# Performance work log

Hardware: AMD Instinct MI355X
Metric: run time of the kernel (lower is better)

## Reference

```python
import jax, jax.numpy as jnp
import numpy as np

N_NODES = 50000
N_EDGES = 800000
N_GRAPHS = 64
IN_C, HID_C, OUT_C = 768, 128, 1


def setup_inputs() -> dict:
    key = jax.random.key(0)
    ks = jax.random.split(key, 9)
    x = jax.random.normal(ks[0], (N_NODES, IN_C), dtype=jnp.float32)
    edge_index = jax.random.randint(ks[1], (2, N_EDGES), 0, N_NODES, dtype=jnp.int32)
    batch = jnp.sort(jax.random.randint(ks[2], (N_NODES,), 0, N_GRAPHS, dtype=jnp.int32))
    s1 = 1.0 / np.sqrt(IN_C)
    s2 = 1.0 / np.sqrt(HID_C)
    W1 = jax.random.normal(ks[3], (IN_C, HID_C), dtype=jnp.float32) * s1
    b1 = jnp.zeros((HID_C,), dtype=jnp.float32)
    W2 = jax.random.normal(ks[4], (HID_C, HID_C), dtype=jnp.float32) * s2
    b2 = jnp.zeros((HID_C,), dtype=jnp.float32)
    Wl = jax.random.normal(ks[5], (HID_C, OUT_C), dtype=jnp.float32) * s2
    bl = jnp.zeros((OUT_C,), dtype=jnp.float32)
    return {"x": x, "edge_index": edge_index, "batch": batch,
            "W1": W1, "b1": b1, "W2": W2, "b2": b2, "Wl": Wl, "bl": bl}


def gcn_conv(x, W, b, src, dst, n_nodes):
    """PyG GCNConv: linear transform, symmetric norm with self-loops, scatter-add."""
    xl = x @ W  # [N, C_out]
    # in-degree including self-loop
    deg = jax.ops.segment_sum(jnp.ones_like(dst, dtype=xl.dtype), dst,
                              num_segments=n_nodes) + 1.0
    dinv = jax.lax.rsqrt(deg)  # deg >= 1 so safe
    norm = dinv[src] * dinv[dst]  # [E]
    agg = jax.ops.segment_sum(norm[:, None] * xl[src], dst, num_segments=n_nodes)
    # self-loop message: dinv[i]^2 * xl[i]
    agg = agg + xl * (dinv * dinv)[:, None]
    return agg + b


def reference(x, edge_index, batch, W1, b1, W2, b2, Wl, bl):
    src, dst = edge_index[0], edge_index[1]
    n = x.shape[0]
    h = jax.nn.relu(gcn_conv(x, W1, b1, src, dst, n))
    # dropout is identity in eval mode
    h = jax.nn.relu(gcn_conv(h, W2, b2, src, dst, n))
    # global mean pool over graphs
    sums = jax.ops.segment_sum(h, batch, num_segments=N_GRAPHS)
    cnts = jax.ops.segment_sum(jnp.ones((n,), dtype=h.dtype), batch,
                               num_segments=N_GRAPHS)
    pooled = sums / jnp.maximum(cnts, 1.0)[:, None]
    return pooled @ Wl + bl
```

## Files before the change

kernel.cpp:

```cpp
#include <hip/hip_runtime.h>

#define N_NODES  50000
#define N_EDGES  800000
#define N_GRAPHS 64
#define N_CHUNK  4
#define ZREP     16
#define SCAN_BLOCKS 196
#define GATHER_BLOCKS 784

typedef unsigned short u16x8 __attribute__((ext_vector_type(8)));
typedef short s16x8 __attribute__((ext_vector_type(8)));
typedef float f32x4 __attribute__((ext_vector_type(4)));

__device__ __forceinline__ float bf2f(unsigned short h) {
    return __uint_as_float((unsigned)h << 16);
}
__device__ __forceinline__ unsigned short f2bf(float f) {
    unsigned u = __float_as_uint(f);
    unsigned r = (u + 0x7FFFu + ((u >> 16) & 1u)) >> 16;
    return (unsigned short)r;
}
__device__ __forceinline__ unsigned pk2(float a, float b) {
    return (unsigned)f2bf(a) | ((unsigned)f2bf(b) << 16);
}


__global__ void zero_int_kernel(int* __restrict__ p, int n) {
    for (int i = blockIdx.x * blockDim.x + threadIdx.x; i < n; i += gridDim.x * blockDim.x)
        p[i] = 0;
}

__global__ void hist_kernel(const int* __restrict__ ei, int* __restrict__ cnt) {
    const int* dst = ei + N_EDGES;
    for (int e = blockIdx.x * blockDim.x + threadIdx.x; e < N_EDGES; e += gridDim.x * blockDim.x)
        atomicAdd(&cnt[dst[e]], 1);
}

__global__ void scanA_kernel(const int* __restrict__ cnt, int* __restrict__ bsum,
                             float* __restrict__ dinv) {
    __shared__ int wsum[4];
    int t = threadIdx.x;
    int i = blockIdx.x * 256 + t;
    int v = cnt[i];
    if (i < N_NODES) dinv[i] = rsqrtf((float)v + 1.f);
    int s = v;
    #pragma unroll
    for (int off = 1; off < 64; off <<= 1) s += __shfl_xor(s, off);
    if ((t & 63) == 0) wsum[t >> 6] = s;
    __syncthreads();
    if (t == 0) bsum[blockIdx.x] = wsum[0] + wsum[1] + wsum[2] + wsum[3];
}

__global__ void scanB_kernel(const int* __restrict__ bsum, int* __restrict__ boff) {
    __shared__ int wsum[4];
    int t = threadIdx.x;
    int lane = t & 63, w = t >> 6;
    int v = (t < SCAN_BLOCKS) ? bsum[t] : 0;
    int s = v;
    #pragma unroll
    for (int off = 1; off < 64; off <<= 1) {
        int u = __shfl_up(s, off);
        if (lane >= off) s += u;
    }
    if (lane == 63) wsum[w] = s;
    __syncthreads();
    int wo = 0;
    for (int j = 0; j < w; ++j) wo += wsum[j];
    if (t < SCAN_BLOCKS) boff[t] = wo + s - v;
}

__global__ void scanC_kernel(int* __restrict__ cnt, const int* __restrict__ boff,
                             int* __restrict__ rowptr) {
    __shared__ int wsum[4];
    int t = threadIdx.x;
    int i = blockIdx.x * 256 + t;
    int lane = t & 63, w = t >> 6;
    int v = cnt[i];
    int s = v;
    #pragma unroll
    for (int off = 1; off < 64; off <<= 1) {
        int u = __shfl_up(s, off);
        if (lane >= off) s += u;
    }
    if (lane == 63) wsum[w] = s;
    __syncthreads();
    int wo = 0;
    for (int j = 0; j < w; ++j) wo += wsum[j];
    rowptr[i] = boff[blockIdx.x] + wo + s - v;
    cnt[i] = 0;
}

__global__ void fill_kernel(const int* __restrict__ ei, const int* __restrict__ rowptr,
                            int* __restrict__ fill, const float* __restrict__ dinv,
                            int2* __restrict__ csr) {
    const int* src = ei;
    const int* dst = ei + N_EDGES;
    for (int e = blockIdx.x * blockDim.x + threadIdx.x; e < N_EDGES; e += gridDim.x * blockDim.x) {
        int s = src[e], d = dst[e];
        int pos = rowptr[d] + atomicAdd(&fill[d], 1);
        csr[pos] = make_int2(s, __float_as_int(dinv[s] * dinv[d]));
    }
}

__global__ void gcount_bs_kernel(const int* __restrict__ batch, float* __restrict__ cntg,
                                 float* __restrict__ zsumR) {
    int g = threadIdx.x;
    if (g >= N_GRAPHS) return;
    #pragma unroll
    for (int r = 0; r < ZREP; ++r) zsumR[r * N_GRAPHS + g] = 0.f;
    int lo = 0, hi = N_NODES;
    while (lo < hi) { int mid = (lo + hi) >> 1; if (batch[mid] < g) lo = mid + 1; else hi = mid; }
    int a = lo;
    lo = 0; hi = N_NODES;
    while (lo < hi) { int mid = (lo + hi) >> 1; if (batch[mid] < g + 1) lo = mid + 1; else hi = mid; }
    cntg[g] = (float)(lo - a);
}

__global__ void prep_w_kernel(const float* __restrict__ W1, const float* __restrict__ W2,
                              unsigned short* __restrict__ w1h, unsigned short* __restrict__ w1l,
                              unsigned short* __restrict__ w2h, unsigned short* __restrict__ w2l) {
    const int n1 = 768 * 128, n2 = 128 * 128;
    for (int i = blockIdx.x * blockDim.x + threadIdx.x; i < n1 + n2; i += gridDim.x * blockDim.x) {
        if (i < n1) {
            int k = i >> 7, c = i & 127;
            float w = W1[i];
            unsigned short hi = f2bf(w);
            unsigned short lo = f2bf(w - bf2f(hi));
            w1h[c * 768 + k] = hi;
            w1l[c * 768 + k] = lo;
        } else {
            int j = i - n1;
            int k = j >> 7, c = j & 127;
            float w = W2[j];
            unsigned short hi = f2bf(w);
            unsigned short lo = f2bf(w - bf2f(hi));
            w2h[c * 128 + k] = hi;
            w2l[c * 128 + k] = lo;
        }
    }
}

template<int K, bool BF16A>
__global__ __launch_bounds__(256) void gemm_mfma(const void* __restrict__ Av,
                                                 const unsigned short* __restrict__ Wth,
                                                 const unsigned short* __restrict__ Wtl,
                                                 unsigned short* __restrict__ C, int M) {
    __shared__ unsigned short Xs[128 * 40];
    __shared__ unsigned short Wh[128 * 40];
    __shared__ unsigned short Wl[128 * 40];

    const int tid  = threadIdx.x;
    const int row0 = blockIdx.x * 128;
    const int trow  = tid >> 1;
    const int thalf = (tid & 1) * 16;

    int grow = row0 + trow;
    if (grow >= M) grow = M - 1;
    const float* xpf = (const float*)Av + (long)grow * K + thalf;
    const unsigned short* xpb = (const unsigned short*)Av + (long)grow * K + thalf;
    const unsigned short* wph = Wth + (long)trow * K + thalf;
    const unsigned short* wpl = Wtl + (long)trow * K + thalf;

    f32x4 acc[8][2];
    #pragma unroll
    for (int rf = 0; rf < 8; ++rf)
        #pragma unroll
        for (int cf = 0; cf < 2; ++cf)
            acc[rf][cf] = (f32x4){0.f, 0.f, 0.f, 0.f};

    float4 f0, f1, f2, f3;
    uint4 b0, b1;
    if constexpr (!BF16A) {
        f0 = *(const float4*)(xpf);
        f1 = *(const float4*)(xpf + 4);
        f2 = *(const float4*)(xpf + 8);
        f3 = *(const float4*)(xpf + 12);
    } else {
        b0 = *(const uint4*)(xpb);
        b1 = *(const uint4*)(xpb + 8);
    }

    const int l   = tid & 63;
    const int wv  = tid >> 6;
    const int lr  = l & 15;
    const int lk8 = (l >> 4) * 8;

    for (int k0 = 0; k0 < K; k0 += 32) {
        uint4 wh0 = ((const uint4*)(wph + k0))[0];
        uint4 wh1 = ((const uint4*)(wph + k0))[1];
        uint4 wl0 = ((const uint4*)(wpl + k0))[0];
        uint4 wl1 = ((const uint4*)(wpl + k0))[1];
        unsigned short* xrow = &Xs[trow * 40 + thalf];
        if constexpr (!BF16A) {
            *(uint4*)(xrow)     = make_uint4(pk2(f0.x, f0.y), pk2(f0.z, f0.w), pk2(f1.x, f1.y), pk2(f1.z, f1.w));
            *(uint4*)(xrow + 8) = make_uint4(pk2(f2.x, f2.y), pk2(f2.z, f2.w), pk2(f3.x, f3.y), pk2(f3.z, f3.w));
        } else {
            *(uint4*)(xrow)     = b0;
            *(uint4*)(xrow + 8) = b1;
        }
        *(uint4*)&Wh[trow * 40 + thalf]     = wh0;
        *(uint4*)&Wh[trow * 40 + thalf + 8] = wh1;
        *(uint4*)&Wl[trow * 40 + thalf]     = wl0;
        *(uint4*)&Wl[trow * 40 + thalf + 8] = wl1;
        __syncthreads();

        if (k0 + 32 < K) {
            if constexpr (!BF16A) {
                f0 = *(const float4*)(xpf + k0 + 32);
                f1 = *(const float4*)(xpf + k0 + 36);
                f2 = *(const float4*)(xpf + k0 + 40);
                f3 = *(const float4*)(xpf + k0 + 44);
            } else {
                b0 = *(const uint4*)(xpb + k0 + 32);
                b1 = *(const uint4*)(xpb + k0 + 40);
            }
        }

        s16x8 xb[8], whf[2], wlf[2];
        #pragma unroll
        for (int rf = 0; rf < 8; ++rf)
            xb[rf] = *(const s16x8*)&Xs[(rf * 16 + lr) * 40 + lk8];
        #pragma unroll
        for (int cf = 0; cf < 2; ++cf) {
            whf[cf] = *(const s16x8*)&Wh[(wv * 32 + cf * 16 + lr) * 40 + lk8];
            wlf[cf] = *(const s16x8*)&Wl[(wv * 32 + cf * 16 + lr) * 40 + lk8];
        }
        #pragma unroll
        for (int rf = 0; rf < 8; ++rf)
            #pragma unroll
            for (int cf = 0; cf < 2; ++cf) {
                acc[rf][cf] = __builtin_amdgcn_mfma_f32_16x16x32_bf16(wlf[cf], xb[rf], acc[rf][cf], 0, 0, 0);
                acc[rf][cf] = __builtin_amdgcn_mfma_f32_16x16x32_bf16(whf[cf], xb[rf], acc[rf][cf], 0, 0, 0);
            }
        __syncthreads();
    }

    const int c4 = (l >> 4) * 4;
    #pragma unroll
    for (int rf = 0; rf < 8; ++rf) {
        int r = row0 + rf * 16 + lr;
        if (r < M) {
            #pragma unroll
            for (int cf = 0; cf < 2; ++cf) {
                int cb = wv * 32 + cf * 16 + c4;
                ushort4 v;
                v.x = f2bf(acc[rf][cf][0]);
                v.y = f2bf(acc[rf][cf][1]);
                v.z = f2bf(acc[rf][cf][2]);
                v.w = f2bf(acc[rf][cf][3]);
                *(ushort4*)(C + ((long)(cb >> 5) * N_NODES + r) * 32 + (cb & 31)) = v;
            }
        }
    }
}

template<int MODE>
__global__ __launch_bounds__(256, 4) void gather_all_kernel(
        const unsigned short* __restrict__ xlc, const float* __restrict__ dinv,
        const int* __restrict__ rowptr, const int2* __restrict__ csr,
        const float* __restrict__ bias, unsigned short* __restrict__ outbuf,
        const float* __restrict__ Wl, const int* __restrict__ batch,
        float* __restrict__ zsumR) {
    const int lane = threadIdx.x & 63;

    const int grp   = blockIdx.x & 7;
    const int chunk = grp & 3;
    const unsigned short* xc = xlc + (long)chunk * N_NODES * 32;

    const int cblk = (blockIdx.x >> 3) + (grp >> 2) * 98;
    const int wvc  = cblk * 4 + (threadIdx.x >> 6);
    const int node = wvc * 64 + lane;
    const bool vn = node < N_NODES;
    const int cnode = vn ? node : N_NODES - 1;

    const int start = rowptr[cnode];
    const int end   = vn ? rowptr[cnode + 1] : start;
    const float di  = dinv[cnode];

    const u16x8* srow = (const u16x8*)(xc + (long)cnode * 32);
    u16x8 s0 = srow[0], s1 = srow[1], s2 = srow[2], s3 = srow[3];

    float acc[32];
    #pragma unroll
    for (int j = 0; j < 32; ++j) acc[j] = 0.f;

    int e = start;
    for (; e + 1 < end; e += 2) {
        int2 cA = csr[e];
        int2 cB = csr[e + 1];
        float wA = __int_as_float(cA.y);
        float wB = __int_as_float(cB.y);
        const u16x8* rA = (const u16x8*)(xc + (long)cA.x * 32);
        const u16x8* rB = (const u16x8*)(xc + (long)cB.x * 32);
        u16x8 a0 = rA[0], a1 = rA[1], a2 = rA[2], a3 = rA[3];
        u16x8 b0 = rB[0], b1 = rB[1], b2 = rB[2], b3 = rB[3];
        #pragma unroll
        for (int j = 0; j < 8; ++j) {
            acc[j]      = fmaf(wA, bf2f(a0[j]), acc[j]);
            acc[j + 8]  = fmaf(wA, bf2f(a1[j]), acc[j + 8]);
            acc[j + 16] = fmaf(wA, bf2f(a2[j]), acc[j + 16]);
            acc[j + 24] = fmaf(wA, bf2f(a3[j]), acc[j + 24]);
        }
        #pragma unroll
        for (int j = 0; j < 8; ++j) {
            acc[j]      = fmaf(wB, bf2f(b0[j]), acc[j]);
            acc[j + 8]  = fmaf(wB, bf2f(b1[j]), acc[j + 8]);
            acc[j + 16] = fmaf(wB, bf2f(b2[j]), acc[j + 16]);
            acc[j + 24] = fmaf(wB, bf2f(b3[j]), acc[j + 24]);
        }
    }
    if (e < end) {
        int2 cA = csr[e];
        float wA = __int_as_float(cA.y);
        const u16x8* rA = (const u16x8*)(xc + (long)cA.x * 32);
        u16x8 a0 = rA[0], a1 = rA[1], a2 = rA[2], a3 = rA[3];
        #pragma unroll
        for (int j = 0; j < 8; ++j) {
            acc[j]      = fmaf(wA, bf2f(a0[j]), acc[j]);
            acc[j + 8]  = fmaf(wA, bf2f(a1[j]), acc[j + 8]);
            acc[j + 16] = fmaf(wA, bf2f(a2[j]), acc[j + 16]);
            acc[j + 24] = fmaf(wA, bf2f(a3[j]), acc[j + 24]);
        }
    }

    const float w2 = di * di;
    const float* bch = bias + chunk * 32;
    float s[32];
    #pragma unroll
    for (int j = 0; j < 8; ++j) {
        s[j]      = fmaxf(fmaf(w2, bf2f(s0[j]), acc[j])      + bch[j],      0.f);
        s[j + 8]  = fmaxf(fmaf(w2, bf2f(s1[j]), acc[j + 8])  + bch[j + 8],  0.f);
        s[j + 16] = fmaxf(fmaf(w2, bf2f(s2[j]), acc[j + 16]) + bch[j + 16], 0.f);
        s[j + 24] = fmaxf(fmaf(w2, bf2f(s3[j]), acc[j + 24]) + bch[j + 24], 0.f);
    }

    if (MODE == 0) {
        if (vn) {
            unsigned short* op = outbuf + (long)node * 128 + chunk * 32;
            u16x8 o0, o1, o2, o3;
            #pragma unroll
            for (int j = 0; j < 8; ++j) {
                o0[j] = f2bf(s[j]);
                o1[j] = f2bf(s[j + 8]);
                o2[j] = f2bf(s[j + 16]);
                o3[j] = f2bf(s[j + 24]);
            }
            ((u16x8*)op)[0] = o0;
            ((u16x8*)op)[1] = o1;
            ((u16x8*)op)[2] = o2;
            ((u16x8*)op)[3] = o3;
        }
    } else {
        const float* wch = Wl + chunk * 32;
        float z = 0.f;
        #pragma unroll
        for (int j = 0; j < 32; ++j) z = fmaf(s[j], wch[j], z);
        if (!vn) z = 0.f;
        int b = batch[cnode];
        int b0v = __shfl(b, 0);
        bool uniform = __all(b == b0v);
        if (uniform) {
            #pragma unroll
            for (int off = 1; off < 64; off <<= 1) z += __shfl_xor(z, off);
            if (lane == 0)
                atomicAdd(&zsumR[(blockIdx.x & (ZREP - 1)) * N_GRAPHS + b0v], z);
        } else if (vn) {
            atomicAdd(&zsumR[(blockIdx.x & (ZREP - 1)) * N_GRAPHS + b], z);
        }
    }
}

__global__ void out_kernel(const float* __restrict__ zsumR, const float* __restrict__ cntg,
                           const float* __restrict__ bl, float* __restrict__ out) {
    int g = threadIdx.x;
    if (g < N_GRAPHS) {
        float z = 0.f;
        #pragma unroll
        for (int r = 0; r < ZREP; ++r) z += zsumR[r * N_GRAPHS + g];
        out[g] = z / fmaxf(cntg[g], 1.f) + bl[0];
    }
}


extern "C" void kernel_launch(void* const* d_in, const int* in_sizes, int n_in,
                              void* d_out, int out_size, void* d_ws, size_t ws_size,
                              hipStream_t stream) {
    const float* x    = (const float*)d_in[0];
    const int*   ei   = (const int*)d_in[1];
    const int*   batch= (const int*)d_in[2];
    const float* W1   = (const float*)d_in[3];
    const float* b1   = (const float*)d_in[4];
    const float* W2   = (const float*)d_in[5];
    const float* b2   = (const float*)d_in[6];
    const float* Wl   = (const float*)d_in[7];
    const float* bl   = (const float*)d_in[8];
    float* out = (float*)d_out;

    float* ws      = (float*)d_ws;
    float* dinv    = ws;
    float* zsumR   = ws + 50176;
    float* cntg    = ws + 51200;
    int*   cnt_i   = (int*)(ws + 51264);
    int*   rowptr  = (int*)(ws + 101440);
    int2*  csr     = (int2*)(ws + 151616);
    unsigned short* xl16 = (unsigned short*)(ws + 1751616);
    unsigned short* h1   = (unsigned short*)(ws + 1751616 + 3200000);
    unsigned short* w1h = (unsigned short*)(ws + 11351616);
    unsigned short* w1l = w1h + 98304;
    unsigned short* w2h = w1l + 98304;
    unsigned short* w2l = w2h + 16384;
    int* bsum = (int*)(w2l + 16384);
    int* boff = bsum + 256;

    zero_int_kernel<<<128, 256, 0, stream>>>(cnt_i, 50176);

    hist_kernel<<<1024, 256, 0, stream>>>(ei, cnt_i);
    scanA_kernel<<<SCAN_BLOCKS, 256, 0, stream>>>(cnt_i, bsum, dinv);
    scanB_kernel<<<1, 256, 0, stream>>>(bsum, boff);
    scanC_kernel<<<SCAN_BLOCKS, 256, 0, stream>>>(cnt_i, boff, rowptr);
    fill_kernel<<<1024, 256, 0, stream>>>(ei, rowptr, cnt_i, dinv, csr);
    gcount_bs_kernel<<<1, 64, 0, stream>>>(batch, cntg, zsumR);
    prep_w_kernel<<<448, 256, 0, stream>>>(W1, W2, w1h, w1l, w2h, w2l);

    gemm_mfma<768, false><<<391, 256, 0, stream>>>(x, w1h, w1l, xl16, N_NODES);
    gather_all_kernel<0><<<GATHER_BLOCKS, 256, 0, stream>>>(
        xl16, dinv, rowptr, csr, b1, h1, nullptr, nullptr, nullptr);

    gemm_mfma<128, true><<<391, 256, 0, stream>>>(h1, w2h, w2l, xl16, N_NODES);
    gather_all_kernel<1><<<GATHER_BLOCKS, 256, 0, stream>>>(
        xl16, dinv, rowptr, csr, b2, nullptr, Wl, batch, zsumR);

    out_kernel<<<1, 64, 0, stream>>>(zsumR, cntg, bl, out);
}
```

Baseline: 279.7 us.

## Sort nodes by degree so gather wavefronts process similar-length neighbor lists

Adds a counting-sort pipeline (per-block degree histogram, two scans, stable rank placement) that builds a permutation of nodes ordered by clamped in-degree. Both gather kernels now map each lane to perm[slot], so lanes in a wavefront share similar loop trip counts and divergence drops. The cost is four extra small kernels. Locality of self-row loads and output writes is also lost, and the pooling step becomes per-lane atomics, since lanes no longer hold contiguous nodes of one graph.

```diff
diff --git a/kernel.cpp b/kernel.cpp
--- a/kernel.cpp
+++ b/kernel.cpp
@@ -99,6 +99,70 @@
         int s = src[e], d = dst[e];
         int pos = rowptr[d] + atomicAdd(&fill[d], 1);
         csr[pos] = make_int2(s, __float_as_int(dinv[s] * dinv[d]));
+    }
+}
+
+__global__ void dhistA_kernel(const int* __restrict__ rowptr, int* __restrict__ bhist) {
+    __shared__ int h[64];
+    int t = threadIdx.x;
+    if (t < 64) h[t] = 0;
+    __syncthreads();
+    int i = blockIdx.x * 256 + t;
+    if (i < N_NODES) {
+        int d = min(rowptr[i + 1] - rowptr[i], 63);
+        atomicAdd(&h[d], 1);
+    }
+    __syncthreads();
+    if (t < 64) bhist[t * SCAN_BLOCKS + blockIdx.x] = h[t];
+}
+
+__global__ void dscanB1_kernel(int* __restrict__ bhist, int* __restrict__ binsum) {
+    __shared__ int wsum[4];
+    int d = blockIdx.x;
+    int t = threadIdx.x;
+    int lane = t & 63, w = t >> 6;
+    int v = (t < SCAN_BLOCKS) ? bhist[d * SCAN_BLOCKS + t] : 0;
+    int s = v;
+    #pragma unroll
+    for (int off = 1; off < 64; off <<= 1) {
+        int u = __shfl_up(s, off);
+        if (lane >= off) s += u;
+    }
+    if (lane == 63) wsum[w] = s;
+    __syncthreads();
+    int wo = 0;
+    for (int j = 0; j < w; ++j) wo += wsum[j];
+    if (t < SCAN_BLOCKS) bhist[d * SCAN_BLOCKS + t] = wo + s - v;
+    if (t == SCAN_BLOCKS - 1) binsum[d] = wo + s;
+}
+
+__global__ void dscanB2_kernel(int* __restrict__ binsum) {
+    int t = threadIdx.x;
+    int v = binsum[t];
+    int s = v;
+    #pragma unroll
+    for (int off = 1; off < 64; off <<= 1) {
+        int u = __shfl_up(s, off);
+        if (t >= off) s += u;
+    }
+    binsum[t] = s - v;
+}
+
+__global__ void dpermC_kernel(const int* __restrict__ rowptr, const int* __restrict__ bhist,
+                              const int* __restrict__ binoff, int* __restrict__ perm) {
+    __shared__ unsigned char degs[256];
+    int t = threadIdx.x;
+    int i = blockIdx.x * 256 + t;
+    bool vi = i < N_NODES;
+    int d = 255;
+    if (vi) d = min(rowptr[i + 1] - rowptr[i], 63);
+    degs[t] = (unsigned char)d;
+    __syncthreads();
+    if (vi) {
+        int rank = 0;
+        for (int j = 0; j < t; ++j) rank += (degs[j] == (unsigned char)d);
+        int pos = binoff[d] + bhist[d * SCAN_BLOCKS + blockIdx.x] + rank;
+        perm[pos] = i;
     }
 }
 
@@ -258,6 +322,7 @@
 __global__ __launch_bounds__(256, 4) void gather_all_kernel(
         const unsigned short* __restrict__ xlc, const float* __restrict__ dinv,
         const int* __restrict__ rowptr, const int2* __restrict__ csr,
+        const int* __restrict__ perm,
         const float* __restrict__ bias, unsigned short* __restrict__ outbuf,
         const float* __restrict__ Wl, const int* __restrict__ batch,
         float* __restrict__ zsumR) {
@@ -269,15 +334,15 @@
 
     const int cblk = (blockIdx.x >> 3) + (grp >> 2) * 98;
     const int wvc  = cblk * 4 + (threadIdx.x >> 6);
-    const int node = wvc * 64 + lane;
-    const bool vn = node < N_NODES;
-    const int cnode = vn ? node : N_NODES - 1;
-
-    const int start = rowptr[cnode];
-    const int end   = vn ? rowptr[cnode + 1] : start;
-    const float di  = dinv[cnode];
-
-    const u16x8* srow = (const u16x8*)(xc + (long)cnode * 32);
+    const int slot = wvc * 64 + lane;
+    const bool vn  = slot < N_NODES;
+    const int node = vn ? perm[slot] : (N_NODES - 1);
+
+    const int start = rowptr[node];
+    const int end   = vn ? rowptr[node + 1] : start;
+    const float di  = dinv[node];
+
+    const u16x8* srow = (const u16x8*)(xc + (long)node * 32);
     u16x8 s0 = srow[0], s1 = srow[1], s2 = srow[2], s3 = srow[3];
 
     float acc[32];
@@ -355,18 +420,8 @@
         float z = 0.f;
         #pragma unroll
         for (int j = 0; j < 32; ++j) z = fmaf(s[j], wch[j], z);
-        if (!vn) z = 0.f;
-        int b = batch[cnode];
-        int b0v = __shfl(b, 0);
-        bool uniform = __all(b == b0v);
-        if (uniform) {
-            #pragma unroll
-            for (int off = 1; off < 64; off <<= 1) z += __shfl_xor(z, off);
-            if (lane == 0)
-                atomicAdd(&zsumR[(blockIdx.x & (ZREP - 1)) * N_GRAPHS + b0v], z);
-        } else if (vn) {
-            atomicAdd(&zsumR[(blockIdx.x & (ZREP - 1)) * N_GRAPHS + b], z);
-        }
+        if (vn)
+            atomicAdd(&zsumR[(lane & (ZREP - 1)) * N_GRAPHS + batch[node]], z);
     }
 }
 
@@ -409,8 +464,11 @@
     unsigned short* w1l = w1h + 98304;
     unsigned short* w2h = w1l + 98304;
     unsigned short* w2l = w2h + 16384;
-    int* bsum = (int*)(w2l + 16384);
-    int* boff = bsum + 256;
+    int* bsum  = (int*)(w2l + 16384);
+    int* boff  = bsum + 256;
+    int* bhist = boff + 256;
+    int* binsum= bhist + 12544;
+    int* perm  = binsum + 64;
 
     zero_int_kernel<<<128, 256, 0, stream>>>(cnt_i, 50176);
 
@@ -419,16 +477,21 @@
     scanB_kernel<<<1, 256, 0, stream>>>(bsum, boff);
     scanC_kernel<<<SCAN_BLOCKS, 256, 0, stream>>>(cnt_i, boff, rowptr);
     fill_kernel<<<1024, 256, 0, stream>>>(ei, rowptr, cnt_i, dinv, csr);
+    dhistA_kernel<<<SCAN_BLOCKS, 256, 0, stream>>>(rowptr, bhist);
+    dscanB1_kernel<<<64, 256, 0, stream>>>(bhist, binsum);
+    dscanB2_kernel<<<1, 64, 0, stream>>>(binsum);
+    dpermC_kernel<<<SCAN_BLOCKS, 256, 0, stream>>>(rowptr, bhist, binsum, perm);
+
     gcount_bs_kernel<<<1, 64, 0, stream>>>(batch, cntg, zsumR);
     prep_w_kernel<<<448, 256, 0, stream>>>(W1, W2, w1h, w1l, w2h, w2l);
 
     gemm_mfma<768, false><<<391, 256, 0, stream>>>(x, w1h, w1l, xl16, N_NODES);
     gather_all_kernel<0><<<GATHER_BLOCKS, 256, 0, stream>>>(
-        xl16, dinv, rowptr, csr, b1, h1, nullptr, nullptr, nullptr);
+        xl16, dinv, rowptr, csr, perm, b1, h1, nullptr, nullptr, nullptr);
 
     gemm_mfma<128, true><<<391, 256, 0, stream>>>(h1, w2h, w2l, xl16, N_NODES);
     gather_all_kernel<1><<<GATHER_BLOCKS, 256, 0, stream>>>(
-        xl16, dinv, rowptr, csr, b2, nullptr, Wl, batch, zsumR);
+        xl16, dinv, rowptr, csr, perm, b2, nullptr, Wl, batch, zsumR);
 
     out_kernel<<<1, 64, 0, stream>>>(zsumR, cntg, bl, out);
 }
```

Result: slower. 341.8 us (+22.2%).

## Split each node's 32-channel gather across two lanes to raise parallelism

Applied to the files above, without the earlier changes.

Each node's 32-channel chunk of the gather is now handled by two adjacent lanes, each covering 16 channels. This halves per-thread registers and accumulators, doubles the gather grid, and raises the occupancy hint in launch bounds. It adds a shuffle to combine the pooled partial dot products, and now spreads atomics over replica slots by lane. The intent is more waves in flight to hide random neighbor-row memory latency, at the cost of duplicated CSR and rowptr loads per lane pair.

```diff
diff --git a/kernel.cpp b/kernel.cpp
--- a/kernel.cpp
+++ b/kernel.cpp
@@ -6,7 +6,7 @@
 #define N_CHUNK  4
 #define ZREP     16
 #define SCAN_BLOCKS 196
-#define GATHER_BLOCKS 784
+#define GATHER_BLOCKS 1568
 
 typedef unsigned short u16x8 __attribute__((ext_vector_type(8)));
 typedef short s16x8 __attribute__((ext_vector_type(8)));
@@ -255,34 +255,36 @@
 }
 
 template<int MODE>
-__global__ __launch_bounds__(256, 4) void gather_all_kernel(
+__global__ __launch_bounds__(256, 6) void gather_all_kernel(
         const unsigned short* __restrict__ xlc, const float* __restrict__ dinv,
         const int* __restrict__ rowptr, const int2* __restrict__ csr,
         const float* __restrict__ bias, unsigned short* __restrict__ outbuf,
         const float* __restrict__ Wl, const int* __restrict__ batch,
         float* __restrict__ zsumR) {
     const int lane = threadIdx.x & 63;
+    const int half = lane & 1;
+    const int c0   = half * 16;
 
     const int grp   = blockIdx.x & 7;
     const int chunk = grp & 3;
     const unsigned short* xc = xlc + (long)chunk * N_NODES * 32;
 
-    const int cblk = (blockIdx.x >> 3) + (grp >> 2) * 98;
+    const int cblk = (blockIdx.x >> 3) + (grp >> 2) * 196;
     const int wvc  = cblk * 4 + (threadIdx.x >> 6);
-    const int node = wvc * 64 + lane;
-    const bool vn = node < N_NODES;
-    const int cnode = vn ? node : N_NODES - 1;
-
-    const int start = rowptr[cnode];
-    const int end   = vn ? rowptr[cnode + 1] : start;
-    const float di  = dinv[cnode];
-
-    const u16x8* srow = (const u16x8*)(xc + (long)cnode * 32);
-    u16x8 s0 = srow[0], s1 = srow[1], s2 = srow[2], s3 = srow[3];
-
-    float acc[32];
-    #pragma unroll
-    for (int j = 0; j < 32; ++j) acc[j] = 0.f;
+    const int slot = wvc * 32 + (lane >> 1);
+    const bool vn  = slot < N_NODES;
+    const int node = vn ? slot : N_NODES - 1;
+
+    const int start = rowptr[node];
+    const int end   = vn ? rowptr[node + 1] : start;
+    const float di  = dinv[node];
+
+    const u16x8* srow = (const u16x8*)(xc + (long)node * 32 + c0);
+    u16x8 s0 = srow[0], s1 = srow[1];
+
+    float acc[16];
+    #pragma unroll
+    for (int j = 0; j < 16; ++j) acc[j] = 0.f;
 
     int e = start;
     for (; e + 1 < end; e += 2) {
@@ -290,73 +292,62 @@
         int2 cB = csr[e + 1];
         float wA = __int_as_float(cA.y);
         float wB = __int_as_float(cB.y);
-        const u16x8* rA = (const u16x8*)(xc + (long)cA.x * 32);
-        const u16x8* rB = (const u16x8*)(xc + (long)cB.x * 32);
-        u16x8 a0 = rA[0], a1 = rA[1], a2 = rA[2], a3 = rA[3];
-        u16x8 b0 = rB[0], b1 = rB[1], b2 = rB[2], b3 = rB[3];
+        const u16x8* rA = (const u16x8*)(xc + (long)cA.x * 32 + c0);
+        const u16x8* rB = (const u16x8*)(xc + (long)cB.x * 32 + c0);
+        u16x8 a0 = rA[0], a1 = rA[1];
+        u16x8 b0 = rB[0], b1 = rB[1];
         #pragma unroll
         for (int j = 0; j < 8; ++j) {
-            acc[j]      = fmaf(wA, bf2f(a0[j]), acc[j]);
-            acc[j + 8]  = fmaf(wA, bf2f(a1[j]), acc[j + 8]);
-            acc[j + 16] = fmaf(wA, bf2f(a2[j]), acc[j + 16]);
-            acc[j + 24] = fmaf(wA, bf2f(a3[j]), acc[j + 24]);
+            acc[j]     = fmaf(wA, bf2f(a0[j]), acc[j]);
+            acc[j + 8] = fmaf(wA, bf2f(a1[j]), acc[j + 8]);
         }
         #pragma unroll
         for (int j = 0; j < 8; ++j) {
-            acc[j]      = fmaf(wB, bf2f(b0[j]), acc[j]);
-            acc[j + 8]  = fmaf(wB, bf2f(b1[j]), acc[j + 8]);
-            acc[j + 16] = fmaf(wB, bf2f(b2[j]), acc[j + 16]);
-            acc[j + 24] = fmaf(wB, bf2f(b3[j]), acc[j + 24]);
+            acc[j]     = fmaf(wB, bf2f(b0[j]), acc[j]);
+            acc[j + 8] = fmaf(wB, bf2f(b1[j]), acc[j + 8]);
         }
     }
     if (e < end) {
         int2 cA = csr[e];
         float wA = __int_as_float(cA.y);
-        const u16x8* rA = (const u16x8*)(xc + (long)cA.x * 32);
-        u16x8 a0 = rA[0], a1 = rA[1], a2 = rA[2], a3 = rA[3];
+        const u16x8* rA = (const u16x8*)(xc + (long)cA.x * 32 + c0);
+        u16x8 a0 = rA[0], a1 = rA[1];
         #pragma unroll
         for (int j = 0; j < 8; ++j) {
-            acc[j]      = fmaf(wA, bf2f(a0[j]), acc[j]);
-            acc[j + 8]  = fmaf(wA, bf2f(a1[j]), acc[j + 8]);
-            acc[j + 16] = fmaf(wA, bf2f(a2[j]), acc[j + 16]);
-            acc[j + 24] = fmaf(wA, bf2f(a3[j]), acc[j + 24]);
+            acc[j]     = fmaf(wA, bf2f(a0[j]), acc[j]);
+            acc[j + 8] = fmaf(wA, bf2f(a1[j]), acc[j + 8]);
         }
     }
 
     const float w2 = di * di;
-    const float* bch = bias + chunk * 32;
-    float s[32];
+    const float* bch = bias + chunk * 32 + c0;
+    float s[16];
     #pragma unroll
     for (int j = 0; j < 8; ++j) {
-        s[j]      = fmaxf(fmaf(w2, bf2f(s0[j]), acc[j])      + bch[j],      0.f);
-        s[j + 8]  = fmaxf(fmaf(w2, bf2f(s1[j]), acc[j + 8])  + bch[j + 8],  0.f);
-        s[j + 16] = fmaxf(fmaf(w2, bf2f(s2[j]), acc[j + 16]) + bch[j + 16], 0.f);
-        s[j + 24] = fmaxf(fmaf(w2, bf2f(s3[j]), acc[j + 24]) + bch[j + 24], 0.f);
+        s[j]     = fmaxf(fmaf(w2, bf2f(s0[j]), acc[j])     + bch[j],     0.f);
+        s[j + 8] = fmaxf(fmaf(w2, bf2f(s1[j]), acc[j + 8]) + bch[j + 8], 0.f);
     }
 
     if (MODE == 0) {
         if (vn) {
-            unsigned short* op = outbuf + (long)node * 128 + chunk * 32;
-            u16x8 o0, o1, o2, o3;
+            unsigned short* op = outbuf + (long)node * 128 + chunk * 32 + c0;
+            u16x8 o0, o1;
             #pragma unroll
             for (int j = 0; j < 8; ++j) {
                 o0[j] = f2bf(s[j]);
                 o1[j] = f2bf(s[j + 8]);
-                o2[j] = f2bf(s[j + 16]);
-                o3[j] = f2bf(s[j + 24]);
             }
             ((u16x8*)op)[0] = o0;
             ((u16x8*)op)[1] = o1;
-            ((u16x8*)op)[2] = o2;
-            ((u16x8*)op)[3] = o3;
         }
     } else {
-        const float* wch = Wl + chunk * 32;
+        const float* wch = Wl + chunk * 32 + c0;
         float z = 0.f;
         #pragma unroll
-        for (int j = 0; j < 32; ++j) z = fmaf(s[j], wch[j], z);
-        if (!vn) z = 0.f;
-        int b = batch[cnode];
+        for (int j = 0; j < 16; ++j) z = fmaf(s[j], wch[j], z);
+        z += __shfl_xor(z, 1);
+        if (!vn || half) z = 0.f;
+        int b = batch[node];
         int b0v = __shfl(b, 0);
         bool uniform = __all(b == b0v);
         if (uniform) {
@@ -364,8 +355,8 @@
             for (int off = 1; off < 64; off <<= 1) z += __shfl_xor(z, off);
             if (lane == 0)
                 atomicAdd(&zsumR[(blockIdx.x & (ZREP - 1)) * N_GRAPHS + b0v], z);
-        } else if (vn) {
-            atomicAdd(&zsumR[(blockIdx.x & (ZREP - 1)) * N_GRAPHS + b], z);
+        } else if (vn && !half) {
+            atomicAdd(&zsumR[((lane >> 1) & (ZREP - 1)) * N_GRAPHS + b], z);
         }
     }
 }
```

Measured after the change: 246.9 us. -11.7%, faster.
